# Performance work log

Hardware: AMD Instinct MI355X
Metric: run time of the kernel (lower is better)

## Reference

```python
import jax, jax.numpy as jnp
import numpy as np
from jax import lax

B, S, D_IN, D_OUT = 2, 1024, 2048, 2048
H, DK, DV, K = 8, 64, 128, 4
CONV_DIM = H * (3 * DK + DV)  # q,k,f each DK per head; v is DV per head
G = H * DV


def _rsa_scan(q, k, v, f, W):
    # q,k,f: [B,S,H,DK]; v: [B,S,H,DV]; W: [H,DV,DV]
    # matrix-valued per-head state St: [B,H,DK,DV], GRU-style gated update
    qs = jnp.moveaxis(q, 1, 0)
    ks = jnp.moveaxis(k, 1, 0)
    vs = jnp.moveaxis(v, 1, 0)
    fs = jnp.moveaxis(f, 1, 0)
    S0 = jnp.zeros((q.shape[0], H, DK, DV), q.dtype)

    def step(St, xs):
        qt, kt, vt, ft = xs
        g = jax.nn.sigmoid(ft)  # [B,H,DK] forget gate
        cand = jnp.tanh(vt[:, :, None, :] + jnp.einsum('bhkv,hvw->bhkw', St, W))
        St = g[..., None] * St + kt[..., None] * cand  # [B,H,DK,DV]
        yt = jnp.einsum('bhk,bhkv->bhv', qt, St)  # readout [B,H,DV]
        return St, yt

    _, ys = lax.scan(step, S0, (qs, ks, vs, fs))
    return jnp.moveaxis(ys, 0, 1)  # [B,S,H,DV]


def setup_inputs() -> dict:
    key = jax.random.key(0)
    ks = jax.random.split(key, 11)
    std = 0.02
    return {
        'x': jax.random.normal(ks[0], (B, S, D_IN), jnp.float32),
        'w_in': jax.random.normal(ks[1], (CONV_DIM + G, D_IN), jnp.float32) * std,
        'b_in': jax.random.normal(ks[2], (CONV_DIM + G,), jnp.float32) * std,
        'conv_w': jax.random.normal(ks[3], (CONV_DIM, 1, K), jnp.float32) * std,
        'conv_b': jax.random.normal(ks[4], (CONV_DIM,), jnp.float32) * std,
        'D': 1.0 + 0.1 * jax.random.normal(ks[5], (H, DV), jnp.float32),
        'state_weight': jax.random.normal(ks[6], (H, DV, DV), jnp.float32) * std,
        'forget_multiplier': 0.1 * jax.random.normal(ks[7], (H,), jnp.float32),
        'forget_bias': 0.1 * jax.random.normal(ks[8], (H, DK), jnp.float32),
        'g_w': 1.0 + 0.1 * jax.random.normal(ks[9], (G,), jnp.float32),
        'w_out': jax.random.normal(ks[10], (D_OUT, G), jnp.float32) * std,
    }


def reference(x, w_in, b_in, conv_w, conv_b, D, state_weight, forget_multiplier, forget_bias, g_w, w_out):
    h = x @ w_in.T + b_in  # input projection [B,S,CONV_DIM+G]
    conv_in, gate = h[..., :CONV_DIM], h[..., CONV_DIM:]
    # causal depthwise conv1d (left pad K-1) + SiLU activation
    xc = jnp.swapaxes(conv_in, 1, 2)  # [B,C,S]
    yc = lax.conv_general_dilated(xc, conv_w, (1,), [(K - 1, 0)], feature_group_count=CONV_DIM)
    yc = jax.nn.silu(yc + conv_b[None, :, None])
    yc = jnp.swapaxes(yc, 1, 2)  # [B,S,CONV_DIM]
    o = 0
    q = yc[..., o:o + H * DK].reshape(B, S, H, DK); o += H * DK
    k = yc[..., o:o + H * DK].reshape(B, S, H, DK); o += H * DK
    v = yc[..., o:o + H * DV].reshape(B, S, H, DV); o += H * DV
    f = yc[..., o:o + H * DK].reshape(B, S, H, DK)
    # p=2 key normalization over head dim (elementwise_affine=False)
    k = k * lax.rsqrt(jnp.sum(k * k, -1, keepdims=True) + 1e-12)
    f = 2.0 * jax.nn.sigmoid(forget_multiplier)[None, None, :, None] * (f + forget_bias[None, None])
    y = _rsa_scan(q, k, v, f, state_weight)  # [B,S,H,DV]
    y = (y + v * D[None, None]).reshape(B, S, G)
    y = y * jax.nn.silu(gate)
    y = y * lax.rsqrt(jnp.mean(y * y, -1, keepdims=True) + 1e-6) * g_w  # RMSNorm
    return y @ w_out.T
```

## Files before the change

kernel.cpp:

```cpp
#include <hip/hip_runtime.h>

typedef unsigned short u16;
typedef unsigned int u32;
typedef __attribute__((ext_vector_type(8))) short short8;
typedef __attribute__((ext_vector_type(4))) float f32x4;

#define N_B 2
#define N_S 1024
#define N_DIN 2048
#define N_DOUT 2048
#define N_H 8
#define N_DK 64
#define N_DV 128
#define N_CONVD 2560
#define N_G 1024
#define N_NH 3584

__device__ __forceinline__ u16 f2bf(float f) {
  u32 u = __float_as_uint(f);
  u32 r = (u + 0x7FFFu + ((u >> 16) & 1u)) >> 16;
  return (u16)r;
}
__device__ __forceinline__ float fsigmoid(float x) {
  return __builtin_amdgcn_rcpf(1.f + __builtin_amdgcn_exp2f(-1.44269504f * x));
}
__device__ __forceinline__ u32 pack_bf16_rhu(float a, float b) {
  u32 ua = __float_as_uint(a) + 0x8000u;
  u32 ub = __float_as_uint(b) + 0x8000u;
  return __builtin_amdgcn_perm(ub, ua, 0x07060302u);
}

__global__ void cvt_kernel(const float* __restrict__ src, u16* __restrict__ dst, int n) {
  int i4 = (blockIdx.x * 256 + threadIdx.x) * 4;
  if (i4 + 3 < n) {
    float4 v = *(const float4*)&src[i4];
    dst[i4 + 0] = f2bf(v.x);
    dst[i4 + 1] = f2bf(v.y);
    dst[i4 + 2] = f2bf(v.z);
    dst[i4 + 3] = f2bf(v.w);
  }
}

__global__ void wtprep_kernel(const float* __restrict__ sw, u16* __restrict__ wtb) {
  int idx = blockIdx.x * 256 + threadIdx.x;
  if (idx >= N_H * 128 * 128) return;
  int h = idx >> 14;
  int rem = idx & 16383;
  int j = rem >> 7, v = rem & 127;
  wtb[idx] = f2bf(sw[((size_t)h * 128 + v) * 128 + j]);
}

__global__ __launch_bounds__(256, 2) void gemm_bt(const u16* __restrict__ A,
                                                  const u16* __restrict__ B,
                                                  const float* __restrict__ bias,
                                                  float* __restrict__ C, int M, int N, int K) {
  const int tid = threadIdx.x;
  const int lane = tid & 63, w = tid >> 6;
  const int u = lane >> 4, m16 = lane & 15;
  const int wm = w & 1, wn = w >> 1;
  const int m0 = blockIdx.y * 128, n0 = blockIdx.x * 128;

  __shared__ __align__(16) u16 As[128 * 32];
  __shared__ __align__(16) u16 Bs[128 * 32];

  f32x4 acc[4][4];
#pragma unroll
  for (int i = 0; i < 4; ++i)
#pragma unroll
    for (int j = 0; j < 4; ++j)
#pragma unroll
      for (int r = 0; r < 4; ++r) acc[i][j][r] = 0.f;

  for (int kk = 0; kk < K; kk += 32) {
#pragma unroll
    for (int q = 0; q < 2; ++q) {
      int chunk = tid + 256 * q;
      int row = chunk >> 2, col = (chunk & 3) * 8;
      *(uint4*)&As[row * 32 + col] = *(const uint4*)&A[(size_t)(m0 + row) * K + kk + col];
      *(uint4*)&Bs[row * 32 + col] = *(const uint4*)&B[(size_t)(n0 + row) * K + kk + col];
    }
    __syncthreads();
    short8 af[4], bfr[4];
#pragma unroll
    for (int i = 0; i < 4; ++i) af[i] = *(const short8*)&As[(64 * wm + 16 * i + m16) * 32 + 8 * u];
#pragma unroll
    for (int i = 0; i < 4; ++i) bfr[i] = *(const short8*)&Bs[(64 * wn + 16 * i + m16) * 32 + 8 * u];
#pragma unroll
    for (int am = 0; am < 4; ++am)
#pragma unroll
      for (int bn = 0; bn < 4; ++bn)
        acc[am][bn] = __builtin_amdgcn_mfma_f32_16x16x32_bf16(af[am], bfr[bn], acc[am][bn], 0, 0, 0);
    __syncthreads();
  }
#pragma unroll
  for (int am = 0; am < 4; ++am)
#pragma unroll
    for (int bn = 0; bn < 4; ++bn) {
      int n = n0 + 64 * wn + 16 * bn + m16;
      float bv = bias ? bias[n] : 0.f;
#pragma unroll
      for (int r = 0; r < 4; ++r) {
        int m = m0 + 64 * wm + 16 * am + 4 * u + r;
        C[(size_t)m * N + n] = acc[am][bn][r] + bv;
      }
    }
}

__global__ void conv_kernel(const float* __restrict__ h, const float* __restrict__ cw,
                            const float* __restrict__ cb, float* __restrict__ SCIN) {
  int gid = blockIdx.x * 256 + threadIdx.x;
  if (gid >= N_B * N_S * N_CONVD) return;
  int c = gid % N_CONVD;
  int bt = gid / N_CONVD;
  int t = bt & 1023, b = bt >> 10;
  float4 wv = *(const float4*)&cw[c * 4];
  const float* wvp = (const float*)&wv;
  float acc = cb[c];
#pragma unroll
  for (int j = 0; j < 4; ++j) {
    int tt = t - 3 + j;
    if (tt >= 0) acc += wvp[j] * h[((size_t)(b * 1024 + tt)) * N_NH + c];
  }
  float yv = acc * fsigmoid(acc);
  int hh, off;
  if (c < 512) { hh = c >> 6; off = c & 63; }
  else if (c < 1024) { int cc = c - 512; hh = cc >> 6; off = 64 + (cc & 63); }
  else if (c < 2048) { int cc = c - 1024; hh = cc >> 7; off = 192 + (cc & 127); }
  else { int cc = c - 2048; hh = cc >> 6; off = 128 + (cc & 63); }
  SCIN[(((size_t)(b * 8 + hh)) * 1024 + t) * 320 + off] = yv;
}

__global__ void prep2_kernel(float* __restrict__ SCIN, const float* __restrict__ fm,
                             const float* __restrict__ fb) {
  int widx = blockIdx.x * 4 + (threadIdx.x >> 6);
  int lane = threadIdx.x & 63;
  int chain = widx >> 10, t = widx & 1023;
  int hh = chain & 7;
  float* base = SCIN + ((size_t)chain * 1024 + t) * 320;
  float kv = base[64 + lane];
  float s = kv * kv;
#pragma unroll
  for (int m = 1; m < 64; m <<= 1) s += __shfl_xor(s, m, 64);
  float inv = __builtin_amdgcn_rsqf(s + 1e-12f);
  base[64 + lane] = kv * inv;
  float fv = base[128 + lane];
  float scale2 = 2.f * fsigmoid(fm[hh]);
  base[128 + lane] = fsigmoid(scale2 * (fv + fb[hh * 64 + lane]));
}

__global__ __launch_bounds__(512, 2) void scan_kernel(const u16* __restrict__ Wtb,
                                                      const float* __restrict__ SCIN,
                                                      float* __restrict__ Ybp) {
  const int tid = threadIdx.x;
  const int lane = tid & 63, wv = tid >> 6;
  const int u = lane >> 4, m16 = lane & 15;
  const int chain = blockIdx.x >> 2;
  const int ig = blockIdx.x & 3;
  const int hh = chain & 7;

  __shared__ __align__(16) u16 Slds[2][16 * 136];

  short8 Wfrag[4];
  {
    const u16* wb = Wtb + ((size_t)hh * 128 + (16 * wv + m16)) * 128 + 8 * u;
#pragma unroll
    for (int kc = 0; kc < 4; ++kc) Wfrag[kc] = *(const short8*)(wb + 32 * kc);
  }

  for (int x = tid; x < 2 * 16 * 136; x += 512) ((u16*)Slds)[x] = 0;

  const float* scin_c = SCIN + (size_t)chain * 1024 * 320;
  float* ybase = Ybp + ((size_t)(chain * 4 + ig)) * 1024 * 128;

  float Sreg[4] = {0.f, 0.f, 0.f, 0.f};

  float qv = scin_c[16 * ig + m16];
  float kv = scin_c[64 + 16 * ig + m16];
  float gv = scin_c[128 + 16 * ig + m16];
  float4 v4 = *(const float4*)&scin_c[192 + 16 * wv + 4 * u];

  __syncthreads();

  for (int t = 0; t < 1024; ++t) {
    const int tn = (t + 1) & 1023;
    const float* pn = scin_c + (size_t)tn * 320;
    float qn = pn[16 * ig + m16];
    float kn = pn[64 + 16 * ig + m16];
    float gn = pn[128 + 16 * ig + m16];
    float4 vn = *(const float4*)&pn[192 + 16 * wv + 4 * u];

    const u16* Sr = Slds[t & 1];
    u16* Sw = Slds[(t + 1) & 1];

    short8 Bfrag[4];
#pragma unroll
    for (int kc = 0; kc < 4; ++kc)
      Bfrag[kc] = *(const short8*)&Sr[m16 * 136 + 32 * kc + 8 * u];

    f32x4 acc0 = {0.f, 0.f, 0.f, 0.f}, acc1 = {0.f, 0.f, 0.f, 0.f};
    acc0 = __builtin_amdgcn_mfma_f32_16x16x32_bf16(Wfrag[0], Bfrag[0], acc0, 0, 0, 0);
    acc1 = __builtin_amdgcn_mfma_f32_16x16x32_bf16(Wfrag[1], Bfrag[1], acc1, 0, 0, 0);
    acc0 = __builtin_amdgcn_mfma_f32_16x16x32_bf16(Wfrag[2], Bfrag[2], acc0, 0, 0, 0);
    acc1 = __builtin_amdgcn_mfma_f32_16x16x32_bf16(Wfrag[3], Bfrag[3], acc1, 0, 0, 0);

    const float* vvp = (const float*)&v4;
    float p[4];
#pragma unroll
    for (int r = 0; r < 4; ++r) {
      float arg = (acc0[r] + acc1[r]) + vvp[r];
      float e = __builtin_amdgcn_exp2f(arg * 2.88539008f);
      float cand = 1.f - 2.f * __builtin_amdgcn_rcpf(e + 1.f);
      Sreg[r] = gv * Sreg[r] + kv * cand;
      p[r] = qv * Sreg[r];
    }

    uint2 pck;
    pck.x = pack_bf16_rhu(Sreg[0], Sreg[1]);
    pck.y = pack_bf16_rhu(Sreg[2], Sreg[3]);
    *(uint2*)&Sw[m16 * 136 + 16 * wv + 4 * u] = pck;

#pragma unroll
    for (int r = 0; r < 4; ++r) {
      float pr = p[r];
      pr += __int_as_float(__builtin_amdgcn_update_dpp(0, __float_as_int(pr), 0x111, 0xF, 0xF, true));
      pr += __int_as_float(__builtin_amdgcn_update_dpp(0, __float_as_int(pr), 0x112, 0xF, 0xF, true));
      pr += __int_as_float(__builtin_amdgcn_update_dpp(0, __float_as_int(pr), 0x114, 0xF, 0xF, true));
      pr += __int_as_float(__builtin_amdgcn_update_dpp(0, __float_as_int(pr), 0x118, 0xF, 0xF, true));
      p[r] = pr;
    }
    if (m16 == 15) {
      f32x4 yo;
      yo[0] = p[0]; yo[1] = p[1]; yo[2] = p[2]; yo[3] = p[3];
      *(f32x4*)(ybase + (size_t)t * 128 + 16 * wv + 4 * u) = yo;
    }

    asm volatile("s_waitcnt lgkmcnt(0)\n\ts_barrier" ::: "memory");

    qv = qn; kv = kn; gv = gn; v4 = vn;
  }
}

__global__ __launch_bounds__(256, 2) void post_kernel(const float* __restrict__ Ybp,
                                                      const float* __restrict__ SCIN,
                                                      const float* __restrict__ h,
                                                      const float* __restrict__ Dp,
                                                      const float* __restrict__ gwv,
                                                      u16* __restrict__ Zb) {
  const int bt = blockIdx.x;
  const int b = bt >> 10, t = bt & 1023;
  const int lane = threadIdx.x & 63, wvi = threadIdx.x >> 6;
  float z[4];
  float ss = 0.f;
#pragma unroll
  for (int c = 0; c < 4; ++c) {
    int j = threadIdx.x + 256 * c;
    int head = j >> 7, dv = j & 127;
    int chain = b * 8 + head;
    float y = 0.f;
#pragma unroll
    for (int igx = 0; igx < 4; ++igx)
      y += Ybp[(((size_t)(chain * 4 + igx)) * 1024 + t) * 128 + dv];
    float v = SCIN[((size_t)chain * 1024 + t) * 320 + 192 + dv];
    float gate = h[((size_t)(b * 1024 + t)) * N_NH + 2560 + j];
    float zz = (y + v * Dp[j]) * (gate * fsigmoid(gate));
    z[c] = zz;
    ss += zz * zz;
  }
#pragma unroll
  for (int m = 1; m < 64; m <<= 1) ss += __shfl_xor(ss, m, 64);
  __shared__ float red[4];
  if (lane == 0) red[wvi] = ss;
  __syncthreads();
  float tot = red[0] + red[1] + red[2] + red[3];
  float scale = __builtin_amdgcn_rsqf(tot * (1.f / 1024.f) + 1e-6f);
#pragma unroll
  for (int c = 0; c < 4; ++c) {
    int j = threadIdx.x + 256 * c;
    Zb[(size_t)(b * 1024 + t) * 1024 + j] = f2bf(z[c] * scale * gwv[j]);
  }
}

extern "C" void kernel_launch(void* const* d_in, const int* in_sizes, int n_in,
                              void* d_out, int out_size, void* d_ws, size_t ws_size,
                              hipStream_t stream) {
  const float* x    = (const float*)d_in[0];
  const float* w_in = (const float*)d_in[1];
  const float* b_in = (const float*)d_in[2];
  const float* cw   = (const float*)d_in[3];
  const float* cb   = (const float*)d_in[4];
  const float* Dp   = (const float*)d_in[5];
  const float* sw   = (const float*)d_in[6];
  const float* fm   = (const float*)d_in[7];
  const float* fb   = (const float*)d_in[8];
  const float* gwv  = (const float*)d_in[9];
  const float* wo   = (const float*)d_in[10];
  float* out = (float*)d_out;

  char* p = (char*)d_ws;
  auto alloc = [&](size_t bytes) {
    char* r = p;
    p += (bytes + 255) & ~(size_t)255;
    return r;
  };
  u16* xb    = (u16*)alloc((size_t)2048 * 2048 * 2);
  u16* wib   = (u16*)alloc((size_t)3584 * 2048 * 2);
  u16* wob   = (u16*)alloc((size_t)2048 * 1024 * 2);
  u16* wtb   = (u16*)alloc((size_t)8 * 128 * 128 * 2);
  float* hbf = (float*)alloc((size_t)2048 * 3584 * 4);
  float* scin= (float*)alloc((size_t)16 * 1024 * 320 * 4);
  float* ybp = (float*)alloc((size_t)64 * 1024 * 128 * 4);
  u16* zb    = (u16*)alloc((size_t)2048 * 1024 * 2);

  cvt_kernel<<<4096, 256, 0, stream>>>(x, xb, 2048 * 2048);
  cvt_kernel<<<7168, 256, 0, stream>>>(w_in, wib, 3584 * 2048);
  cvt_kernel<<<2048, 256, 0, stream>>>(wo, wob, 2048 * 1024);
  wtprep_kernel<<<512, 256, 0, stream>>>(sw, wtb);

  gemm_bt<<<dim3(3584 / 128, 2048 / 128), 256, 0, stream>>>(xb, wib, b_in, hbf, 2048, 3584, 2048);

  conv_kernel<<<(N_B * N_S * N_CONVD) / 256, 256, 0, stream>>>(hbf, cw, cb, scin);
  prep2_kernel<<<(16 * 1024) / 4, 256, 0, stream>>>(scin, fm, fb);

  scan_kernel<<<64, 512, 0, stream>>>(wtb, scin, ybp);

  post_kernel<<<2048, 256, 0, stream>>>(ybp, scin, hbf, Dp, gwv, zb);

  gemm_bt<<<dim3(2048 / 128, 2048 / 128), 256, 0, stream>>>(zb, wob, nullptr, out, 2048, 2048, 1024);
}
```

Before: 647.1 us.

## Fuse conv with key-norm/forget prep, interleave scan inputs, fold tanh scale, use LDS-direct loads

Merges the conv and prep2 kernels into one per-(chain,t) kernel, which removes a launch and a read-modify-write pass over SCIN. SCIN is relaid so q, k and g sit interleaved in one float4 per lane, and v is moved to offset 256. The tanh scale is pre-folded into the state weights and v, and v is placed into the MFMA accumulator init, which removes per-step adds and multiplies in the scan; post compensates with an inverse scale on D. The GEMM now stages tiles with global_load_lds direct-to-LDS loads instead of loading through registers, which adds some risk around ordering and LDS layout.

Result: slower. 663.4 us (+2.5%).

```diff
diff --git a/kernel.cpp b/kernel.cpp
--- a/kernel.cpp
+++ b/kernel.cpp
@@ -16,6 +16,9 @@
 #define N_G 1024
 #define N_NH 3584
 
+#define TANH_SCALE 2.8853901817f
+#define INV_TANH_SCALE 0.34657359f
+
 __device__ __forceinline__ u16 f2bf(float f) {
   u32 u = __float_as_uint(f);
   u32 r = (u + 0x7FFFu + ((u >> 16) & 1u)) >> 16;
@@ -28,6 +31,10 @@
   u32 ua = __float_as_uint(a) + 0x8000u;
   u32 ub = __float_as_uint(b) + 0x8000u;
   return __builtin_amdgcn_perm(ub, ua, 0x07060302u);
+}
+__device__ __forceinline__ void gll16(const void* g, void* l) {
+  __builtin_amdgcn_global_load_lds((const __attribute__((address_space(1))) u32*)g,
+                                   (__attribute__((address_space(3))) u32*)l, 16, 0, 0);
 }
 
 __global__ void cvt_kernel(const float* __restrict__ src, u16* __restrict__ dst, int n) {
@@ -47,7 +54,7 @@
   int h = idx >> 14;
   int rem = idx & 16383;
   int j = rem >> 7, v = rem & 127;
-  wtb[idx] = f2bf(sw[((size_t)h * 128 + v) * 128 + j]);
+  wtb[idx] = f2bf(TANH_SCALE * sw[((size_t)h * 128 + v) * 128 + j]);
 }
 
 __global__ __launch_bounds__(256, 2) void gemm_bt(const u16* __restrict__ A,
@@ -71,13 +78,14 @@
 #pragma unroll
       for (int r = 0; r < 4; ++r) acc[i][j][r] = 0.f;
 
+  const int row0 = tid >> 2, col0 = (tid & 3) * 8;
   for (int kk = 0; kk < K; kk += 32) {
 #pragma unroll
     for (int q = 0; q < 2; ++q) {
       int chunk = tid + 256 * q;
-      int row = chunk >> 2, col = (chunk & 3) * 8;
-      *(uint4*)&As[row * 32 + col] = *(const uint4*)&A[(size_t)(m0 + row) * K + kk + col];
-      *(uint4*)&Bs[row * 32 + col] = *(const uint4*)&B[(size_t)(n0 + row) * K + kk + col];
+      int row = row0 + 64 * q;
+      gll16(&A[(size_t)(m0 + row) * K + kk + col0], &As[chunk * 8]);
+      gll16(&B[(size_t)(n0 + row) * K + kk + col0], &Bs[chunk * 8]);
     }
     __syncthreads();
     short8 af[4], bfr[4];
@@ -106,46 +114,46 @@
     }
 }
 
-__global__ void conv_kernel(const float* __restrict__ h, const float* __restrict__ cw,
-                            const float* __restrict__ cb, float* __restrict__ SCIN) {
-  int gid = blockIdx.x * 256 + threadIdx.x;
-  if (gid >= N_B * N_S * N_CONVD) return;
-  int c = gid % N_CONVD;
-  int bt = gid / N_CONVD;
-  int t = bt & 1023, b = bt >> 10;
-  float4 wv = *(const float4*)&cw[c * 4];
-  const float* wvp = (const float*)&wv;
+__global__ __launch_bounds__(320, 4) void conv_kernel(const float* __restrict__ h,
+                                                      const float* __restrict__ cw,
+                                                      const float* __restrict__ cb,
+                                                      const float* __restrict__ fm,
+                                                      const float* __restrict__ fb,
+                                                      float* __restrict__ SCIN) {
+  const int bid = blockIdx.x;
+  const int t = bid & 1023, chain = bid >> 10;
+  const int b = chain >> 3, hh = chain & 7;
+  const int tid = threadIdx.x;
+
+  int c, outoff;
+  if (tid < 64) { c = hh * 64 + tid; outoff = tid * 4; }
+  else if (tid < 128) { int i = tid - 64; c = 512 + hh * 64 + i; outoff = i * 4 + 1; }
+  else if (tid < 192) { int i = tid - 128; c = 2048 + hh * 64 + i; outoff = i * 4 + 2; }
+  else { int j = tid - 192; c = 1024 + hh * 128 + j; outoff = 256 + j; }
+
+  float4 w4 = *(const float4*)&cw[c * 4];
+  const float* wp = (const float*)&w4;
   float acc = cb[c];
+  const float* hrow = h + ((size_t)(b * 1024 + t)) * N_NH + c;
 #pragma unroll
   for (int j = 0; j < 4; ++j) {
     int tt = t - 3 + j;
-    if (tt >= 0) acc += wvp[j] * h[((size_t)(b * 1024 + tt)) * N_NH + c];
+    if (tt >= 0) acc += wp[j] * hrow[(ptrdiff_t)(j - 3) * N_NH];
   }
   float yv = acc * fsigmoid(acc);
-  int hh, off;
-  if (c < 512) { hh = c >> 6; off = c & 63; }
-  else if (c < 1024) { int cc = c - 512; hh = cc >> 6; off = 64 + (cc & 63); }
-  else if (c < 2048) { int cc = c - 1024; hh = cc >> 7; off = 192 + (cc & 127); }
-  else { int cc = c - 2048; hh = cc >> 6; off = 128 + (cc & 63); }
-  SCIN[(((size_t)(b * 8 + hh)) * 1024 + t) * 320 + off] = yv;
-}
-
-__global__ void prep2_kernel(float* __restrict__ SCIN, const float* __restrict__ fm,
-                             const float* __restrict__ fb) {
-  int widx = blockIdx.x * 4 + (threadIdx.x >> 6);
-  int lane = threadIdx.x & 63;
-  int chain = widx >> 10, t = widx & 1023;
-  int hh = chain & 7;
-  float* base = SCIN + ((size_t)chain * 1024 + t) * 320;
-  float kv = base[64 + lane];
-  float s = kv * kv;
-#pragma unroll
-  for (int m = 1; m < 64; m <<= 1) s += __shfl_xor(s, m, 64);
-  float inv = __builtin_amdgcn_rsqf(s + 1e-12f);
-  base[64 + lane] = kv * inv;
-  float fv = base[128 + lane];
-  float scale2 = 2.f * fsigmoid(fm[hh]);
-  base[128 + lane] = fsigmoid(scale2 * (fv + fb[hh * 64 + lane]));
+
+  if (tid >= 64 && tid < 128) {
+    float s = yv * yv;
+#pragma unroll
+    for (int m = 1; m < 64; m <<= 1) s += __shfl_xor(s, m, 64);
+    yv *= __builtin_amdgcn_rsqf(s + 1e-12f);
+  } else if (tid >= 128 && tid < 192) {
+    float scale2 = 2.f * fsigmoid(fm[hh]);
+    yv = fsigmoid(scale2 * (yv + fb[hh * 64 + (tid - 128)]));
+  } else if (tid >= 192) {
+    yv *= TANH_SCALE;
+  }
+  SCIN[(size_t)bid * 384 + outoff] = yv;
 }
 
 __global__ __launch_bounds__(512, 2) void scan_kernel(const u16* __restrict__ Wtb,
@@ -169,25 +177,21 @@
 
   for (int x = tid; x < 2 * 16 * 136; x += 512) ((u16*)Slds)[x] = 0;
 
-  const float* scin_c = SCIN + (size_t)chain * 1024 * 320;
+  const float* scin_c = SCIN + (size_t)chain * 1024 * 384;
   float* ybase = Ybp + ((size_t)(chain * 4 + ig)) * 1024 * 128;
 
   float Sreg[4] = {0.f, 0.f, 0.f, 0.f};
 
-  float qv = scin_c[16 * ig + m16];
-  float kv = scin_c[64 + 16 * ig + m16];
-  float gv = scin_c[128 + 16 * ig + m16];
-  float4 v4 = *(const float4*)&scin_c[192 + 16 * wv + 4 * u];
+  float4 qkg = *(const float4*)&scin_c[(16 * ig + m16) * 4];
+  float4 v4 = *(const float4*)&scin_c[256 + 16 * wv + 4 * u];
 
   __syncthreads();
 
   for (int t = 0; t < 1024; ++t) {
     const int tn = (t + 1) & 1023;
-    const float* pn = scin_c + (size_t)tn * 320;
-    float qn = pn[16 * ig + m16];
-    float kn = pn[64 + 16 * ig + m16];
-    float gn = pn[128 + 16 * ig + m16];
-    float4 vn = *(const float4*)&pn[192 + 16 * wv + 4 * u];
+    const float* pn = scin_c + (size_t)tn * 384;
+    float4 qkgn = *(const float4*)&pn[(16 * ig + m16) * 4];
+    float4 vn = *(const float4*)&pn[256 + 16 * wv + 4 * u];
 
     const u16* Sr = Slds[t & 1];
     u16* Sw = Slds[(t + 1) & 1];
@@ -197,18 +201,19 @@
     for (int kc = 0; kc < 4; ++kc)
       Bfrag[kc] = *(const short8*)&Sr[m16 * 136 + 32 * kc + 8 * u];
 
-    f32x4 acc0 = {0.f, 0.f, 0.f, 0.f}, acc1 = {0.f, 0.f, 0.f, 0.f};
+    f32x4 acc0, acc1 = {0.f, 0.f, 0.f, 0.f};
+    acc0[0] = v4.x; acc0[1] = v4.y; acc0[2] = v4.z; acc0[3] = v4.w;
     acc0 = __builtin_amdgcn_mfma_f32_16x16x32_bf16(Wfrag[0], Bfrag[0], acc0, 0, 0, 0);
     acc1 = __builtin_amdgcn_mfma_f32_16x16x32_bf16(Wfrag[1], Bfrag[1], acc1, 0, 0, 0);
     acc0 = __builtin_amdgcn_mfma_f32_16x16x32_bf16(Wfrag[2], Bfrag[2], acc0, 0, 0, 0);
     acc1 = __builtin_amdgcn_mfma_f32_16x16x32_bf16(Wfrag[3], Bfrag[3], acc1, 0, 0, 0);
 
-    const float* vvp = (const float*)&v4;
+    const float qv = qkg.x, kv = qkg.y, gv = qkg.z;
     float p[4];
 #pragma unroll
     for (int r = 0; r < 4; ++r) {
-      float arg = (acc0[r] + acc1[r]) + vvp[r];
-      float e = __builtin_amdgcn_exp2f(arg * 2.88539008f);
+      float arg = acc0[r] + acc1[r];
+      float e = __builtin_amdgcn_exp2f(arg);
       float cand = 1.f - 2.f * __builtin_amdgcn_rcpf(e + 1.f);
       Sreg[r] = gv * Sreg[r] + kv * cand;
       p[r] = qv * Sreg[r];
@@ -236,7 +241,7 @@
 
     asm volatile("s_waitcnt lgkmcnt(0)\n\ts_barrier" ::: "memory");
 
-    qv = qn; kv = kn; gv = gn; v4 = vn;
+    qkg = qkgn; v4 = vn;
   }
 }
 
@@ -260,9 +265,9 @@
 #pragma unroll
     for (int igx = 0; igx < 4; ++igx)
       y += Ybp[(((size_t)(chain * 4 + igx)) * 1024 + t) * 128 + dv];
-    float v = SCIN[((size_t)chain * 1024 + t) * 320 + 192 + dv];
+    float v = SCIN[((size_t)chain * 1024 + t) * 384 + 256 + dv];
     float gate = h[((size_t)(b * 1024 + t)) * N_NH + 2560 + j];
-    float zz = (y + v * Dp[j]) * (gate * fsigmoid(gate));
+    float zz = (y + v * (Dp[j] * INV_TANH_SCALE)) * (gate * fsigmoid(gate));
     z[c] = zz;
     ss += zz * zz;
   }
@@ -307,7 +312,7 @@
   u16* wob   = (u16*)alloc((size_t)2048 * 1024 * 2);
   u16* wtb   = (u16*)alloc((size_t)8 * 128 * 128 * 2);
   float* hbf = (float*)alloc((size_t)2048 * 3584 * 4);
-  float* scin= (float*)alloc((size_t)16 * 1024 * 320 * 4);
+  float* scin= (float*)alloc((size_t)16 * 1024 * 384 * 4);
   float* ybp = (float*)alloc((size_t)64 * 1024 * 128 * 4);
   u16* zb    = (u16*)alloc((size_t)2048 * 1024 * 2);
 
@@ -318,8 +323,7 @@
 
   gemm_bt<<<dim3(3584 / 128, 2048 / 128), 256, 0, stream>>>(xb, wib, b_in, hbf, 2048, 3584, 2048);
 
-  conv_kernel<<<(N_B * N_S * N_CONVD) / 256, 256, 0, stream>>>(hbf, cw, cb, scin);
-  prep2_kernel<<<(16 * 1024) / 4, 256, 0, stream>>>(scin, fm, fb);
+  conv_kernel<<<16 * 1024, 320, 0, stream>>>(hbf, cw, cb, fm, fb, scin);
 
   scan_kernel<<<64, 512, 0, stream>>>(wtb, scin, ybp);
 
```
